# Kernel tuning notes

Measured on AMD Instinct MI355X. Metric: run time of the kernel, lower is better.

The kernel has to match this reference:

```python
import jax, jax.numpy as jnp
import numpy as np

EPS = 1e-12
SMOOTH = 9.0
SGR_STEPS = 3


def l2norm(x, axis=-1):
    return x / jnp.maximum(jnp.linalg.norm(x, axis=axis, keepdims=True), EPS)


def setup_inputs() -> dict:
    key = jax.random.key(0)
    d, s = 1024, 256
    n_img, n_cap, L, n_tok = 64, 64, 32, 197  # 197 -> CLS + 14x14 grid

    def xavier(k, shape):
        lim = float(np.sqrt(6.0 / (shape[-2] + shape[-1])))
        return jax.random.uniform(k, shape, jnp.float32, -lim, lim)

    ks = iter(jax.random.split(key, 32))
    inp = {
        "img_embs": jax.random.normal(next(ks), (n_img, n_tok, d), jnp.float32),
        "cap_embs": jax.random.normal(next(ks), (n_cap, L, d), jnp.float32),
        # constant lengths == max length so the vectorized reference matches
        # the original per-caption loop exactly
        "cap_lens": jnp.full((n_cap,), L, dtype=jnp.int32),
        # visual GlobalSelfAttention
        "vG_Wl": xavier(next(ks), (d, d)), "vG_bl": jnp.zeros((d,), jnp.float32),
        "vG_Wg": xavier(next(ks), (d, d)), "vG_bg": jnp.zeros((d,), jnp.float32),
        "vG_Wc": xavier(next(ks), (d, 1)), "vG_bc": jnp.zeros((1,), jnp.float32),
        # textual GlobalSelfAttention
        "tG_Wl": xavier(next(ks), (d, d)), "tG_bl": jnp.zeros((d,), jnp.float32),
        "tG_Wg": xavier(next(ks), (d, d)), "tG_bg": jnp.zeros((d,), jnp.float32),
        "tG_Wc": xavier(next(ks), (d, 1)), "tG_bc": jnp.zeros((1,), jnp.float32),
        # similarity projections
        "W_loc": xavier(next(ks), (d, s)), "b_loc": jnp.zeros((s,), jnp.float32),
        "W_glo": xavier(next(ks), (d, s)), "b_glo": jnp.zeros((s,), jnp.float32),
        "W_eval": xavier(next(ks), (s, 1)), "b_eval": jnp.zeros((1,), jnp.float32),
        # 3 stacked GraphReasoning layers
        "sgr_Wq": xavier(next(ks), (SGR_STEPS, s, s)), "sgr_bq": jnp.zeros((SGR_STEPS, s), jnp.float32),
        "sgr_Wk": xavier(next(ks), (SGR_STEPS, s, s)), "sgr_bk": jnp.zeros((SGR_STEPS, s), jnp.float32),
        "sgr_Wg": xavier(next(ks), (SGR_STEPS, s, s)), "sgr_bg": jnp.zeros((SGR_STEPS, s), jnp.float32),
    }
    return inp


def global_self_attention(local, raw_global, Wl, bl, Wg, bg, Wc, bc):
    # local: (B, N, d), raw_global: (B, d); dropout is identity at eval
    le = jnp.tanh(local @ Wl + bl)
    ge = jnp.tanh(raw_global @ Wg + bg)
    logits = ((le * ge[:, None, :]) @ Wc + bc)[..., 0]  # (B, N)
    weights = jax.nn.softmax(logits, axis=1)
    global_feat = jnp.sum(weights[..., None] * local, axis=1)
    return l2norm(global_feat, axis=-1)


def scan_attention(query, context, smooth=SMOOTH):
    # query: (B, Nq, d), context: (B, Nc, d)
    attn = jnp.einsum("bcd,bqd->bcq", context, query)
    attn = jax.nn.leaky_relu(attn, negative_slope=0.1)
    attn = l2norm(attn, axis=2)                    # normalize over query dim
    attn = jnp.swapaxes(attn, 1, 2)                # (B, Nq, Nc)
    attn = jax.nn.softmax(attn * smooth, axis=2)   # softmax over context
    weighted = jnp.einsum("bqc,bcd->bqd", attn, context)
    return l2norm(weighted, axis=-1)


def graph_reasoning(sim_emb, Wq, bq, Wk, bk, Wg, bg):
    q = sim_emb @ Wq + bq
    k = sim_emb @ Wk + bk
    edge = jax.nn.softmax(jnp.einsum("bnd,bmd->bnm", q, k), axis=-1)
    sgr = jnp.einsum("bnm,bmd->bnd", edge, sim_emb)
    return jax.nn.relu(sgr @ Wg + bg)


def reference(img_embs, cap_embs, cap_lens,
              vG_Wl, vG_bl, vG_Wg, vG_bg, vG_Wc, vG_bc,
              tG_Wl, tG_bl, tG_Wg, tG_bg, tG_Wc, tG_bc,
              W_loc, b_loc, W_glo, b_glo, W_eval, b_eval,
              sgr_Wq, sgr_bq, sgr_Wk, sgr_bk, sgr_Wg, sgr_bg):
    # 197 tokens -> strip CLS (has_cls_token is True)
    img_tokens = img_embs[:, 1:, :]                      # (n_img, 196, d)
    n_img = img_tokens.shape[0]
    img_avg = img_tokens.mean(axis=1)
    img_global = global_self_attention(img_tokens, img_avg,
                                       vG_Wl, vG_bl, vG_Wg, vG_bg, vG_Wc, vG_bc)

    def per_caption(cap_i):                              # cap_i: (L, d)
        L, d = cap_i.shape
        cap_e = jnp.broadcast_to(cap_i[None], (n_img, L, d))
        cap_avg = jnp.broadcast_to(cap_i.mean(axis=0)[None], (n_img, d))
        cap_global = global_self_attention(cap_e, cap_avg,
                                           tG_Wl, tG_bl, tG_Wg, tG_bg, tG_Wc, tG_bc)
        ctx = scan_attention(cap_e, img_tokens)          # (n_img, L, d)
        sim_loc = l2norm((ctx - cap_e) ** 2 @ W_loc + b_loc, axis=-1)
        sim_glo = l2norm((img_global - cap_global) ** 2 @ W_glo + b_glo, axis=-1)
        sim_emb = jnp.concatenate([sim_glo[:, None, :], sim_loc], axis=1)
        for t in range(SGR_STEPS):
            sim_emb = graph_reasoning(sim_emb, sgr_Wq[t], sgr_bq[t],
                                      sgr_Wk[t], sgr_bk[t], sgr_Wg[t], sgr_bg[t])
        return jax.nn.sigmoid(sim_emb[:, 0, :] @ W_eval + b_eval)[:, 0]  # (n_img,)

    sims = jax.vmap(per_caption)(cap_embs)               # (n_cap, n_img)
    return sims.T                                        # (n_img, n_cap)
```

## Files before the change

### kernel.cpp

```cpp
#include <hip/hip_runtime.h>
#include <hip/hip_bf16.h>
#include <math.h>

#define NI 64
#define NC 64
#define NTOK 197
#define TT 196
#define CL 32
#define DD 1024
#define SS 256
#define NN 33
#define EPSN 1e-12f
#define SMOOTHF 9.0f
#define TP 224

typedef __attribute__((ext_vector_type(8))) short bfrag;
typedef __attribute__((ext_vector_type(4))) float f32x4;
#define MFMA(a, b, c) __builtin_amdgcn_mfma_f32_16x16x32_bf16((a), (b), (c), 0, 0, 0)

#define OFF_ATTNT  0
#define OFF_WTILE  14848
#define OFF_WMAX   23552
#define OFF_NRMS   24064
#define OFF_SEA    0
#define OFF_R1     25344
#define OFF_EB     34560
#define OFF_WKQ    41472
#define OFF_VBUF   42496
#define OFF_QN     42640
#define OFF_RNQ    43152
#define SMEM_BYTES 43280

__device__ __forceinline__ float warp_reduce_sum64(float v) {
#pragma unroll
  for (int m = 32; m > 0; m >>= 1) v += __shfl_xor(v, m, 64);
  return v;
}
__device__ __forceinline__ unsigned short f2b(float f) {
  __hip_bfloat16 h = __float2bfloat16(f);
  return *reinterpret_cast<unsigned short*>(&h);
}
__device__ __forceinline__ float b2f(unsigned short u) {
  union { unsigned int i; float f; } v;
  v.i = ((unsigned int)u) << 16;
  return v.f;
}

__global__ void k_avg(const float* __restrict__ img, const float* __restrict__ cap,
                      float* __restrict__ img_avg, float* __restrict__ cap_avg) {
  int bid = blockIdx.x;
  int tid = threadIdx.x;
  if (bid < NI) {
    int b = bid;
    for (int d = tid; d < DD; d += 256) {
      float acc = 0.f;
      const float* p = img + ((size_t)b * NTOK + 1) * DD + d;
      for (int t = 0; t < TT; ++t) acc += p[(size_t)t * DD];
      img_avg[b * DD + d] = acc * (1.0f / TT);
    }
  } else {
    int c = bid - NI;
    for (int d = tid; d < DD; d += 256) {
      float acc = 0.f;
      const float* p = cap + (size_t)c * CL * DD + d;
      for (int t = 0; t < CL; ++t) acc += p[(size_t)t * DD];
      cap_avg[c * DD + d] = acc * (1.0f / CL);
    }
  }
}

__global__ void k_hvec(const float* __restrict__ avg, const float* __restrict__ Wg,
                       const float* __restrict__ bg, const float* __restrict__ Wc,
                       float* __restrict__ h) {
  __shared__ float av[DD];
  int b = blockIdx.x >> 2;
  int dc = blockIdx.x & 3;
  int tid = threadIdx.x;
  for (int i = tid; i < DD; i += 256) av[i] = avg[b * DD + i];
  __syncthreads();
  int d = dc * 256 + tid;
  float acc = 0.f;
  for (int k = 0; k < DD; k += 4) {
    float4 a4 = *(const float4*)&av[k];
    acc += a4.x * Wg[(size_t)(k + 0) * DD + d];
    acc += a4.y * Wg[(size_t)(k + 1) * DD + d];
    acc += a4.z * Wg[(size_t)(k + 2) * DD + d];
    acc += a4.w * Wg[(size_t)(k + 3) * DD + d];
  }
  h[b * DD + d] = tanhf(acc + bg[d]) * Wc[d];
}

__global__ void k_logits_mfma(const unsigned short* __restrict__ Abf, int rowsPerBatch,
                              const unsigned short* __restrict__ WT,
                              const float* __restrict__ bl, const float* __restrict__ h,
                              float* __restrict__ partial) {
  int tid = threadIdx.x;
  int lane = tid & 63, w = tid >> 6;
  int lrow = lane & 15, lk = (lane >> 4) * 8, rsub = (lane >> 4) * 4;
  int rb = blockIdx.x * 64, c0 = blockIdx.y * 64;
  const unsigned short* ap = Abf + (size_t)(rb + w * 16 + lrow) * DD;
  f32x4 acc[4] = {};
  for (int k0 = 0; k0 < DD; k0 += 32) {
    bfrag a = *(const bfrag*)(ap + k0 + lk);
#pragma unroll
    for (int i = 0; i < 4; ++i) {
      bfrag bb = *(const bfrag*)(WT + (size_t)(c0 + i * 16 + lrow) * DD + k0 + lk);
      acc[i] = MFMA(a, bb, acc[i]);
    }
  }
#pragma unroll
  for (int r = 0; r < 4; ++r) {
    int row = rb + w * 16 + rsub + r;
    int bb2 = row / rowsPerBatch;
    float s = 0.f;
#pragma unroll
    for (int i = 0; i < 4; ++i) {
      int col = c0 + i * 16 + lrow;
      s += tanhf(acc[i][r] + bl[col]) * h[bb2 * DD + col];
    }
    s += __shfl_xor(s, 1, 64);
    s += __shfl_xor(s, 2, 64);
    s += __shfl_xor(s, 4, 64);
    s += __shfl_xor(s, 8, 64);
    if (lrow == 0) partial[(size_t)row * 16 + blockIdx.y] = s;
  }
}

__global__ void k_finish_global(const float* __restrict__ partial, const float* __restrict__ bc,
                                const float* __restrict__ Xbase, long batchStride, int R,
                                float* __restrict__ outG) {
  __shared__ float w[200];
  __shared__ float red[8];
  int b = blockIdx.x, tid = threadIdx.x;
  for (int t = tid; t < R; t += 256) {
    const float* pp = &partial[((size_t)b * R + t) * 16];
    float s = bc[0];
#pragma unroll
    for (int u = 0; u < 16; ++u) s += pp[u];
    w[t] = s;
  }
  __syncthreads();
  float m = -1e30f;
  for (int t = tid; t < R; t += 256) m = fmaxf(m, w[t]);
#pragma unroll
  for (int mm = 32; mm; mm >>= 1) m = fmaxf(m, __shfl_xor(m, mm, 64));
  if ((tid & 63) == 0) red[tid >> 6] = m;
  __syncthreads();
  m = fmaxf(fmaxf(red[0], red[1]), fmaxf(red[2], red[3]));
  __syncthreads();
  for (int t = tid; t < R; t += 256) w[t] = expf(w[t] - m);
  __syncthreads();
  const float* xb = Xbase + (size_t)b * batchStride;
  float acc[4];
  float ss = 0.f;
#pragma unroll
  for (int c4 = 0; c4 < 4; ++c4) {
    int d = tid + c4 * 256;
    float a = 0.f;
    for (int t = 0; t < R; ++t) a += w[t] * xb[(size_t)t * DD + d];
    acc[c4] = a;
    ss += a * a;
  }
  ss = warp_reduce_sum64(ss);
  if ((tid & 63) == 0) red[tid >> 6] = ss;
  __syncthreads();
  ss = red[0] + red[1] + red[2] + red[3];
  float rn = 1.0f / fmaxf(sqrtf(ss), EPSN);
#pragma unroll
  for (int c4 = 0; c4 < 4; ++c4) outG[(size_t)b * DD + tid + c4 * 256] = acc[c4] * rn;
}

__global__ void k_simglo(const float* __restrict__ ig, const float* __restrict__ cg,
                         const float* __restrict__ W, const float* __restrict__ bgl,
                         float* __restrict__ simglo) {
  __shared__ float a_lds[32][20];
  __shared__ float b_lds[32][260];
  int tid = threadIdx.x;
  int p0 = blockIdx.x * 16;
  int ty = tid >> 6, tx = tid & 63;
  int s_rr = tid >> 3, s_kq = tid & 7;
  float acc[4][4] = {};
  for (int k0 = 0; k0 < DD; k0 += 32) {
    float d2[4] = {};
    if (tid < 128) {
      int p = p0 + s_rr;
      int b = p >> 6, c = p & 63;
      float4 giv = *(const float4*)&ig[b * DD + k0 + s_kq * 4];
      float4 cgv = *(const float4*)&cg[c * DD + k0 + s_kq * 4];
      float dx = giv.x - cgv.x, dy = giv.y - cgv.y, dz = giv.z - cgv.z, dw = giv.w - cgv.w;
      d2[0] = dx * dx; d2[1] = dy * dy; d2[2] = dz * dz; d2[3] = dw * dw;
    }
    float4 wv[8];
#pragma unroll
    for (int u = 0; u < 8; ++u)
      wv[u] = *(const float4*)&W[(size_t)(k0 + s_rr) * SS + s_kq * 32 + u * 4];
    __syncthreads();
    if (tid < 128) {
#pragma unroll
      for (int u = 0; u < 4; ++u) a_lds[s_kq * 4 + u][s_rr] = d2[u];
    }
#pragma unroll
    for (int u = 0; u < 8; ++u)
      *(float4*)&b_lds[s_rr][s_kq * 32 + u * 4] = wv[u];
    __syncthreads();
#pragma unroll
    for (int kk = 0; kk < 32; ++kk) {
      float4 a4 = *(const float4*)&a_lds[kk][ty * 4];
      float4 b4 = *(const float4*)&b_lds[kk][tx * 4];
      float av[4] = {a4.x, a4.y, a4.z, a4.w};
      float bv[4] = {b4.x, b4.y, b4.z, b4.w};
#pragma unroll
      for (int i = 0; i < 4; ++i)
#pragma unroll
        for (int j = 0; j < 4; ++j) acc[i][j] += av[i] * bv[j];
    }
  }
#pragma unroll
  for (int i = 0; i < 4; ++i) {
    float v[4];
    float ssq = 0.f;
#pragma unroll
    for (int j = 0; j < 4; ++j) {
      v[j] = acc[i][j] + bgl[tx * 4 + j];
      ssq += v[j] * v[j];
    }
    ssq = warp_reduce_sum64(ssq);
    float rn = 1.0f / fmaxf(sqrtf(ssq), EPSN);
    int p = p0 + ty * 4 + i;
    *(float4*)&simglo[(size_t)p * SS + tx * 4] =
        make_float4(v[0] * rn, v[1] * rn, v[2] * rn, v[3] * rn);
  }
}

__global__ void k_mmatb(const float* __restrict__ Wa, const float* __restrict__ Wb,
                        unsigned short* __restrict__ M) {
  __shared__ float a_lds[32][68];
  __shared__ float b_lds[32][68];
  int tid = threadIdx.x;
  int t = blockIdx.x >> 4;
  int dt = (blockIdx.x >> 2) & 3, et = blockIdx.x & 3;
  int d0 = dt * 64, e0 = et * 64;
  const float* wq = Wa + (size_t)t * SS * SS;
  const float* wk = Wb + (size_t)t * SS * SS;
  int ty = tid >> 4, tx = tid & 15;
  int s_rr = tid >> 2, s_kq = tid & 3;
  float acc[4][4] = {};
  for (int j0 = 0; j0 < SS; j0 += 32) {
    float4 q0 = *(const float4*)&wq[(size_t)(d0 + s_rr) * SS + j0 + s_kq * 8];
    float4 q1 = *(const float4*)&wq[(size_t)(d0 + s_rr) * SS + j0 + s_kq * 8 + 4];
    float4 k0v = *(const float4*)&wk[(size_t)(e0 + s_rr) * SS + j0 + s_kq * 8];
    float4 k1v = *(const float4*)&wk[(size_t)(e0 + s_rr) * SS + j0 + s_kq * 8 + 4];
    __syncthreads();
    float qa[8] = {q0.x, q0.y, q0.z, q0.w, q1.x, q1.y, q1.z, q1.w};
    float ka[8] = {k0v.x, k0v.y, k0v.z, k0v.w, k1v.x, k1v.y, k1v.z, k1v.w};
#pragma unroll
    for (int u = 0; u < 8; ++u) {
      a_lds[s_kq * 8 + u][s_rr] = qa[u];
      b_lds[s_kq * 8 + u][s_rr] = ka[u];
    }
    __syncthreads();
#pragma unroll
    for (int kk = 0; kk < 32; ++kk) {
      float4 a4 = *(const float4*)&a_lds[kk][ty * 4];
      float4 b4 = *(const float4*)&b_lds[kk][tx * 4];
      float av[4] = {a4.x, a4.y, a4.z, a4.w};
      float bv[4] = {b4.x, b4.y, b4.z, b4.w};
#pragma unroll
      for (int i = 0; i < 4; ++i)
#pragma unroll
        for (int j = 0; j < 4; ++j) acc[i][j] += av[i] * bv[j];
    }
  }
#pragma unroll
  for (int i = 0; i < 4; ++i) {
    unsigned int lo = (unsigned int)f2b(acc[i][0]) | ((unsigned int)f2b(acc[i][1]) << 16);
    unsigned int hi = (unsigned int)f2b(acc[i][2]) | ((unsigned int)f2b(acc[i][3]) << 16);
    uint2 o = make_uint2(lo, hi);
    *(uint2*)(M + (size_t)t * SS * SS + (size_t)(d0 + ty * 4 + i) * SS + e0 + tx * 4) = o;
  }
}

__global__ void k_wkbq(const float* __restrict__ Wk, const float* __restrict__ bq,
                       float* __restrict__ out) {
  __shared__ float bv[SS];
  int t = blockIdx.x, tid = threadIdx.x;
  const float* wk = Wk + (size_t)t * SS * SS;
  bv[tid] = bq[t * SS + tid];
  __syncthreads();
  float acc = 0.f;
  for (int j = 0; j < SS; j += 4) {
    float4 wv = *(const float4*)&wk[(size_t)tid * SS + j];
    float4 b4 = *(const float4*)&bv[j];
    acc += wv.x * b4.x + wv.y * b4.y + wv.z * b4.z + wv.w * b4.w;
  }
  out[t * SS + tid] = acc;
}

__global__ void k_imgprep(const float* __restrict__ img, unsigned short* __restrict__ row_bf,
                          unsigned short* __restrict__ tr_bf) {
  __shared__ float t[32][33];
  int b = blockIdx.z;
  int t0 = blockIdx.y * 32, d0 = blockIdx.x * 32;
  int tx = threadIdx.x & 31, ty = threadIdx.x >> 5;
#pragma unroll
  for (int u = 0; u < 4; ++u) {
    int tt = t0 + ty + u * 8;
    float v = (tt < TT) ? img[((size_t)b * NTOK + 1 + tt) * DD + d0 + tx] : 0.f;
    t[ty + u * 8][tx] = v;
    if (tt < TT) row_bf[((size_t)b * TT + tt) * DD + d0 + tx] = f2b(v);
  }
  __syncthreads();
#pragma unroll
  for (int u = 0; u < 4; ++u)
    tr_bf[((size_t)b * DD + d0 + ty + u * 8) * TP + t0 + tx] = f2b(t[tx][ty + u * 8]);
}

__global__ void k_gram_mfma(const unsigned short* __restrict__ img_bf,
                            unsigned short* __restrict__ gram) {
  int tid = threadIdx.x;
  int lane = tid & 63, w = tid >> 6;
  int lrow = lane & 15, lk = (lane >> 4) * 8, rsub = (lane >> 4) * 4;
  int bimg = blockIdx.x;
  int rb = blockIdx.y * 64, cb = blockIdx.z * 64;
  const unsigned short* X = img_bf + (size_t)bimg * TT * DD;
  int ra = rb + w * 16 + lrow;
  if (ra > TT - 1) ra = TT - 1;
  f32x4 acc[4] = {};
  for (int k0 = 0; k0 < DD; k0 += 32) {
    bfrag a = *(const bfrag*)(X + (size_t)ra * DD + k0 + lk);
#pragma unroll
    for (int i = 0; i < 4; ++i) {
      int cc = cb + i * 16 + lrow;
      if (cc > TT - 1) cc = TT - 1;
      bfrag bb = *(const bfrag*)(X + (size_t)cc * DD + k0 + lk);
      acc[i] = MFMA(a, bb, acc[i]);
    }
  }
  unsigned short* Gp = gram + (size_t)bimg * 208 * TP;
#pragma unroll
  for (int i = 0; i < 4; ++i) {
    int cc = cb + i * 16 + lrow;
#pragma unroll
    for (int r = 0; r < 4; ++r) {
      int rr = rb + w * 16 + rsub + r;
      if (rr < 208 && cc < TP)
        Gp[(size_t)rr * TP + cc] = (rr < TT && cc < TT) ? f2b(acc[i][r]) : 0;
    }
  }
}

__global__ void k_castb(const float* __restrict__ s, unsigned short* __restrict__ d, int n4) {
  int i = blockIdx.x * 256 + threadIdx.x;
  if (i < n4) {
    float4 v = *(const float4*)(s + (size_t)i * 4);
    uint2 o;
    o.x = (unsigned int)f2b(v.x) | ((unsigned int)f2b(v.y) << 16);
    o.y = (unsigned int)f2b(v.z) | ((unsigned int)f2b(v.w) << 16);
    *(uint2*)(d + (size_t)i * 4) = o;
  }
}

__global__ void k_tcast(const float* __restrict__ src, unsigned short* __restrict__ dst,
                        int R, int C, long sB, long dB) {
  __shared__ float t[32][33];
  const float* s = src + (size_t)blockIdx.z * sB;
  unsigned short* d = dst + (size_t)blockIdx.z * dB;
  int r0 = blockIdx.y * 32, c0 = blockIdx.x * 32;
  int tx = threadIdx.x & 31, ty = threadIdx.x >> 5;
#pragma unroll
  for (int u = 0; u < 4; ++u)
    t[ty + u * 8][tx] = s[(size_t)(r0 + ty + u * 8) * C + c0 + tx];
  __syncthreads();
#pragma unroll
  for (int u = 0; u < 4; ++u)
    d[(size_t)(c0 + ty + u * 8) * R + r0 + tx] = f2b(t[tx][ty + u * 8]);
}

__global__ __launch_bounds__(256, 3) void k_pair(
    const float* __restrict__ b_loc, const float* __restrict__ simglo,
    const float* __restrict__ wkbq, const float* __restrict__ bg3,
    const float* __restrict__ W_eval, const float* __restrict__ b_eval,
    const unsigned short* __restrict__ cap_bf, const unsigned short* __restrict__ img_bf,
    const unsigned short* __restrict__ imgT_bf, const unsigned short* __restrict__ gram_bf,
    const unsigned short* __restrict__ wlocT_bf, const unsigned short* __restrict__ mt_bf,
    const unsigned short* __restrict__ wgT_bf, float* __restrict__ out) {
  extern __shared__ char smem[];

  int tid = threadIdx.x;
  int lane = tid & 63, w = tid >> 6;
  int lrow = lane & 15;
  int lk = (lane >> 4) * 8;
  int rsub = (lane >> 4) * 4;
  int p = blockIdx.x;
  int b = p >> 6, c = p & 63;
  const unsigned short* imgR = img_bf + (size_t)b * TT * DD;
  const unsigned short* capB = cap_bf + (size_t)c * CL * DD;
  char* attnT_b = smem + OFF_ATTNT;

  {
    f32x4 acc[4][2] = {};
    for (int k0 = 0; k0 < DD; k0 += 32) {
      bfrag bq0 = *(const bfrag*)(capB + (size_t)lrow * DD + k0 + lk);
      bfrag bq1 = *(const bfrag*)(capB + (size_t)(16 + lrow) * DD + k0 + lk);
#pragma unroll
      for (int i = 0; i < 4; ++i) {
        int tt = w + 4 * i;
        if (tt < 13) {
          int t = tt * 16 + lrow;
          bfrag a = {0, 0, 0, 0, 0, 0, 0, 0};
          if (t < TT) a = *(const bfrag*)(imgR + (size_t)t * DD + k0 + lk);
          acc[i][0] = MFMA(a, bq0, acc[i][0]);
          acc[i][1] = MFMA(a, bq1, acc[i][1]);
        }
      }
    }
    float mx0 = -1e30f, mx1 = -1e30f;
#pragma unroll
    for (int i = 0; i < 4; ++i) {
      int tt = w + 4 * i;
      if (tt < 13) {
#pragma unroll
        for (int r = 0; r < 4; ++r) {
          int t = tt * 16 + rsub + r;
          float v0 = acc[i][0][r];
          v0 = v0 < 0.f ? 0.1f * v0 : v0;
          float v1 = acc[i][1][r];
          v1 = v1 < 0.f ? 0.1f * v1 : v1;
          float s2 = v0 * v0 + v1 * v1;
          s2 += __shfl_xor(s2, 1, 64);
          s2 += __shfl_xor(s2, 2, 64);
          s2 += __shfl_xor(s2, 4, 64);
          s2 += __shfl_xor(s2, 8, 64);
          float rn = 1.0f / fmaxf(sqrtf(s2), EPSN);
          v0 *= rn;
          v1 *= rn;
          acc[i][0][r] = v0;
          acc[i][1][r] = v1;
          if (t < TT) {
            mx0 = fmaxf(mx0, v0);
            mx1 = fmaxf(mx1, v1);
          }
        }
      }
    }
    mx0 = fmaxf(mx0, __shfl_xor(mx0, 16, 64));
    mx0 = fmaxf(mx0, __shfl_xor(mx0, 32, 64));
    mx1 = fmaxf(mx1, __shfl_xor(mx1, 16, 64));
    mx1 = fmaxf(mx1, __shfl_xor(mx1, 32, 64));
    float* wmax = (float*)(smem + OFF_WMAX);
    if ((lane >> 4) == 0) {
      wmax[w * 32 + lrow] = mx0;
      wmax[w * 32 + 16 + lrow] = mx1;
    }
    __syncthreads();
    mx0 = fmaxf(fmaxf(wmax[lrow], wmax[32 + lrow]), fmaxf(wmax[64 + lrow], wmax[96 + lrow]));
    mx1 = fmaxf(fmaxf(wmax[16 + lrow], wmax[48 + lrow]),
                fmaxf(wmax[80 + lrow], wmax[112 + lrow]));
#pragma unroll
    for (int i = 0; i < 4; ++i) {
      int tt = w + 4 * i;
#pragma unroll
      for (int r = 0; r < 4; ++r) {
        int t = tt * 16 + rsub + r;
        if (t < TP) {
          unsigned short e0 = 0, e1 = 0;
          if (t < TT) {
            e0 = f2b(expf(SMOOTHF * (acc[i][0][r] - mx0)));
            e1 = f2b(expf(SMOOTHF * (acc[i][1][r] - mx1)));
          }
          *(unsigned short*)(attnT_b + lrow * 464 + t * 2) = e0;
          *(unsigned short*)(attnT_b + (16 + lrow) * 464 + t * 2) = e1;
        }
      }
    }
  }
  __syncthreads();

  {
    float* qn = (float*)(smem + OFF_QN);
    float* nrmS = (float*)(smem + OFF_NRMS);
    const unsigned short* gb = gram_bf + (size_t)b * 208 * TP;
    float part0 = 0.f, part1 = 0.f;
#pragma unroll
    for (int i = 0; i < 4; ++i) {
      int tt = w + 4 * i;
      if (tt < 13) {
        f32x4 y0 = {0.f, 0.f, 0.f, 0.f}, y1 = {0.f, 0.f, 0.f, 0.f};
        for (int t0 = 0; t0 < TP; t0 += 32) {
          bfrag a = *(const bfrag*)(gb + (size_t)(tt * 16 + lrow) * TP + t0 + lk);
          bfrag b0 = *(const bfrag*)(attnT_b + lrow * 464 + (t0 + lk) * 2);
          bfrag b1 = *(const bfrag*)(attnT_b + (16 + lrow) * 464 + (t0 + lk) * 2);
          y0 = MFMA(a, b0, y0);
          y1 = MFMA(a, b1, y1);
        }
#pragma unroll
        for (int r = 0; r < 4; ++r) {
          int t = tt * 16 + rsub + r;
          if (t < TT) {
            part0 += y0[r] * b2f(*(const unsigned short*)(attnT_b + lrow * 464 + t * 2));
            part1 += y1[r] * b2f(*(const unsigned short*)(attnT_b + (16 + lrow) * 464 + t * 2));
          }
        }
      }
    }
    part0 += __shfl_xor(part0, 16, 64);
    part0 += __shfl_xor(part0, 32, 64);
    part1 += __shfl_xor(part1, 16, 64);
    part1 += __shfl_xor(part1, 32, 64);
    if ((lane >> 4) == 0) {
      qn[w * 32 + lrow] = part0;
      qn[w * 32 + 16 + lrow] = part1;
    }
    __syncthreads();
    if (tid < 32)
      nrmS[tid] = 1.0f / fmaxf(sqrtf(qn[tid] + qn[32 + tid] + qn[64 + tid] + qn[96 + tid]), EPSN);
    __syncthreads();
  }

  f32x4 accW[2][4] = {};
  {
    char* wtile_b = smem + OFF_WTILE;
    float* nrmS = (float*)(smem + OFF_NRMS);
    float nrm0 = nrmS[lrow], nrm1 = nrmS[16 + lrow];
    for (int d0 = 0; d0 < DD; d0 += 128) {
      f32x4 c2[2][2] = {};
      for (int t0 = 0; t0 < TP; t0 += 32) {
        bfrag b0 = *(const bfrag*)(attnT_b + lrow * 464 + (t0 + lk) * 2);
        bfrag b1 = *(const bfrag*)(attnT_b + (16 + lrow) * 464 + (t0 + lk) * 2);
#pragma unroll
        for (int i = 0; i < 2; ++i) {
          int dt = w + 4 * i;
          bfrag a = *(const bfrag*)(imgT_bf + ((size_t)b * DD + d0 + dt * 16 + lrow) * TP + t0 + lk);
          c2[i][0] = MFMA(a, b0, c2[i][0]);
          c2[i][1] = MFMA(a, b1, c2[i][1]);
        }
      }
      __syncthreads();
#pragma unroll
      for (int i = 0; i < 2; ++i) {
        int dl = (w + 4 * i) * 16 + rsub;
#pragma unroll
        for (int qt = 0; qt < 2; ++qt) {
          int q = qt * 16 + lrow;
          uint2 cu = *(const uint2*)(capB + (size_t)q * DD + d0 + dl);
          float cf0 = b2f(cu.x & 0xffff), cf1 = b2f(cu.x >> 16);
          float cf2 = b2f(cu.y & 0xffff), cf3 = b2f(cu.y >> 16);
          float rn = qt ? nrm1 : nrm0;
          float v0 = c2[i][qt][0] * rn - cf0;
          float v1 = c2[i][qt][1] * rn - cf1;
          float v2 = c2[i][qt][2] * rn - cf2;
          float v3 = c2[i][qt][3] * rn - cf3;
          unsigned int lo = (unsigned int)f2b(v0 * v0) | ((unsigned int)f2b(v1 * v1) << 16);
          unsigned int hi = (unsigned int)f2b(v2 * v2) | ((unsigned int)f2b(v3 * v3) << 16);
          *(uint2*)(wtile_b + q * 272 + dl * 2) = make_uint2(lo, hi);
        }
      }
      __syncthreads();
      for (int kc = 0; kc < 4; ++kc) {
        bfrag a0 = *(const bfrag*)(wtile_b + lrow * 272 + (kc * 32 + lk) * 2);
        bfrag a1 = *(const bfrag*)(wtile_b + (16 + lrow) * 272 + (kc * 32 + lk) * 2);
#pragma unroll
        for (int sti = 0; sti < 4; ++sti) {
          int s = (w * 4 + sti) * 16 + lrow;
          bfrag bb = *(const bfrag*)(wlocT_bf + (size_t)s * DD + d0 + kc * 32 + lk);
          accW[0][sti] = MFMA(a0, bb, accW[0][sti]);
          accW[1][sti] = MFMA(a1, bb, accW[1][sti]);
        }
      }
    }
  }

  {
    char* seA_b = smem + OFF_SEA;
    float* qn = (float*)(smem + OFF_QN);
    float* rnq = (float*)(smem + OFF_RNQ);
    __syncthreads();
    for (int i2 = tid; i2 < 6336; i2 += 256) ((unsigned int*)smem)[i2] = 0;
    __syncthreads();
    float blv[4];
#pragma unroll
    for (int sti = 0; sti < 4; ++sti) blv[sti] = b_loc[(w * 4 + sti) * 16 + lrow];
    float ss[2][4];
#pragma unroll
    for (int qt = 0; qt < 2; ++qt)
#pragma unroll
      for (int r = 0; r < 4; ++r) {
        float s2 = 0.f;
#pragma unroll
        for (int sti = 0; sti < 4; ++sti) {
          float v = accW[qt][sti][r] + blv[sti];
          s2 += v * v;
        }
        s2 += __shfl_xor(s2, 1, 64);
        s2 += __shfl_xor(s2, 2, 64);
        s2 += __shfl_xor(s2, 4, 64);
        s2 += __shfl_xor(s2, 8, 64);
        ss[qt][r] = s2;
      }
    if (lrow == 0) {
#pragma unroll
      for (int qt = 0; qt < 2; ++qt)
#pragma unroll
        for (int r = 0; r < 4; ++r)
          qn[w * 32 + qt * 16 + rsub + r] = ss[qt][r];
    }
    __syncthreads();
    if (tid < 32)
      rnq[tid] = 1.0f / fmaxf(sqrtf(qn[tid] + qn[32 + tid] + qn[64 + tid] + qn[96 + tid]), EPSN);
    __syncthreads();
#pragma unroll
    for (int qt = 0; qt < 2; ++qt)
#pragma unroll
      for (int r = 0; r < 4; ++r) {
        int q = qt * 16 + rsub + r;
        float rn = rnq[q];
#pragma unroll
        for (int sti = 0; sti < 4; ++sti) {
          int s = (w * 4 + sti) * 16 + lrow;
          float v = (accW[qt][sti][r] + blv[sti]) * rn;
          *(unsigned short*)(seA_b + (1 + q) * 528 + s * 2) = f2b(v);
        }
      }
    if (tid < 64) {
      float4 g4 = *(const float4*)&simglo[(size_t)p * SS + tid * 4];
      unsigned int lo = (unsigned int)f2b(g4.x) | ((unsigned int)f2b(g4.y) << 16);
      unsigned int hi = (unsigned int)f2b(g4.z) | ((unsigned int)f2b(g4.w) << 16);
      *(uint2*)(seA_b + tid * 8) = make_uint2(lo, hi);
    }
    __syncthreads();
  }

  {
    char* seA_b = smem + OFF_SEA;
    char* Gc_b = smem + OFF_R1;
    char* XT_b = smem + OFF_R1;
    float* Ef = (float*)(smem + OFF_R1);
    char* Eb = smem + OFF_EB;
    float* wkq = (float*)(smem + OFF_WKQ);
    float* vbuf = (float*)(smem + OFF_VBUF);

    for (int step = 0; step < 3; ++step) {
      const unsigned short* mstep = mt_bf + (size_t)step * SS * SS;
      const unsigned short* wstep = wgT_bf + (size_t)step * SS * SS;
      wkq[tid] = wkbq[step * SS + tid];
      __syncthreads();
      if (tid < 132) {
        int m = tid >> 2, qq = tid & 3;
        float a = 0.f;
        for (int e = qq * 64; e < qq * 64 + 64; e += 2) {
          unsigned int u = *(const unsigned int*)(seA_b + m * 528 + e * 2);
          a += b2f(u & 0xffff) * wkq[e] + b2f(u >> 16) * wkq[e + 1];
        }
        a += __shfl_xor(a, 1, 64);
        a += __shfl_xor(a, 2, 64);
        if (qq == 0) vbuf[m] = a;
      }
      f32x4 aE[3] = {};
      for (int ec = 0; ec < 4; ++ec) {
        f32x4 aGc[3] = {};
        for (int kc = 0; kc < 8; ++kc) {
          int k = kc * 32 + lk;
          bfrag bb = *(const bfrag*)(mstep + (size_t)(ec * 64 + w * 16 + lrow) * SS + k);
#pragma unroll
          for (int mt = 0; mt < 3; ++mt) {
            bfrag af = *(const bfrag*)(seA_b + (mt * 16 + lrow) * 528 + k * 2);
            aGc[mt] = MFMA(af, bb, aGc[mt]);
          }
        }
        __syncthreads();
#pragma unroll
        for (int mt = 0; mt < 3; ++mt)
#pragma unroll
          for (int r = 0; r < 4; ++r)
            *(unsigned short*)(Gc_b + (mt * 16 + rsub + r) * 144 + (w * 16 + lrow) * 2) =
                f2b(aGc[mt][r]);
        __syncthreads();
#pragma unroll
        for (int kc = 0; kc < 2; ++kc) {
          int k = kc * 32 + lk;
#pragma unroll
          for (int ti = 0; ti < 3; ++ti) {
            int tile = w + ti * 4;
            if (tile < 9) {
              int mtE = tile / 3, ntE = tile - mtE * 3;
              bfrag ga = *(const bfrag*)(Gc_b + (mtE * 16 + lrow) * 144 + k * 2);
              bfrag sb = *(const bfrag*)(seA_b + (ntE * 16 + lrow) * 528 + (ec * 64 + k) * 2);
              aE[ti] = MFMA(ga, sb, aE[ti]);
            }
          }
        }
      }
      __syncthreads();
#pragma unroll
      for (int ti = 0; ti < 3; ++ti) {
        int tile = w + ti * 4;
        if (tile < 9) {
          int mtE = tile / 3, ntE = tile - mtE * 3;
          int n0 = mtE * 16 + rsub, m = ntE * 16 + lrow;
#pragma unroll
          for (int r = 0; r < 4; ++r)
            if (n0 + r < NN && m < NN) Ef[(n0 + r) * 34 + m] = aE[ti][r] + vbuf[m];
        }
      }
      __syncthreads();
      if (tid < NN) {
        float mx = -1e30f;
        for (int mm = 0; mm < NN; ++mm) mx = fmaxf(mx, Ef[tid * 34 + mm]);
        float sum = 0.f;
        for (int mm = 0; mm < NN; ++mm) {
          float e = expf(Ef[tid * 34 + mm] - mx);
          Ef[tid * 34 + mm] = e;
          sum += e;
        }
        float rs = 1.0f / sum;
        for (int mm = 0; mm < NN; ++mm) Ef[tid * 34 + mm] *= rs;
      }
      __syncthreads();
      for (int idx = tid; idx < 48 * 36; idx += 256) {
        int n = idx / 36, mp = (idx - n * 36) * 2;
        unsigned int lo = (n < NN && mp < NN) ? (unsigned int)f2b(Ef[n * 34 + mp]) : 0u;
        unsigned int hi = (n < NN && mp + 1 < NN) ? (unsigned int)f2b(Ef[n * 34 + mp + 1]) : 0u;
        *(unsigned int*)(Eb + n * 144 + mp * 2) = lo | (hi << 16);
      }
      __syncthreads();
      unsigned int oPk[4][3][2];
#pragma unroll
      for (int sc = 0; sc < 4; ++sc) {
        f32x4 aX[3] = {};
        for (int kc = 0; kc < 8; ++kc) {
          int k = kc * 32 + lk;
          bfrag bb = *(const bfrag*)(wstep + (size_t)(sc * 64 + w * 16 + lrow) * SS + k);
#pragma unroll
          for (int mt = 0; mt < 3; ++mt) {
            bfrag af = *(const bfrag*)(seA_b + (mt * 16 + lrow) * 528 + k * 2);
            aX[mt] = MFMA(af, bb, aX[mt]);
          }
        }
        __syncthreads();
#pragma unroll
        for (int mt = 0; mt < 3; ++mt) {
          unsigned int lo = (unsigned int)f2b(aX[mt][0]) | ((unsigned int)f2b(aX[mt][1]) << 16);
          unsigned int hi = (unsigned int)f2b(aX[mt][2]) | ((unsigned int)f2b(aX[mt][3]) << 16);
          *(uint2*)(XT_b + (w * 16 + lrow) * 144 + (mt * 16 + rsub) * 2) = make_uint2(lo, hi);
        }
        *(uint2*)(XT_b + (w * 16 + lrow) * 144 + (48 + rsub) * 2) = make_uint2(0, 0);
        __syncthreads();
        f32x4 aO[3] = {};
#pragma unroll
        for (int kc = 0; kc < 2; ++kc) {
          int k = kc * 32 + lk;
          bfrag xa = *(const bfrag*)(XT_b + (w * 16 + lrow) * 144 + k * 2);
#pragma unroll
          for (int nt = 0; nt < 3; ++nt) {
            bfrag eb = *(const bfrag*)(Eb + (nt * 16 + lrow) * 144 + k * 2);
            aO[nt] = MFMA(xa, eb, aO[nt]);
          }
        }
        float bga[4];
#pragma unroll
        for (int r = 0; r < 4; ++r) bga[r] = bg3[step * SS + sc * 64 + w * 16 + rsub + r];
#pragma unroll
        for (int nt = 0; nt < 3; ++nt) {
          float v0 = fmaxf(aO[nt][0] + bga[0], 0.f);
          float v1 = fmaxf(aO[nt][1] + bga[1], 0.f);
          float v2 = fmaxf(aO[nt][2] + bga[2], 0.f);
          float v3 = fmaxf(aO[nt][3] + bga[3], 0.f);
          oPk[sc][nt][0] = (unsigned int)f2b(v0) | ((unsigned int)f2b(v1) << 16);
          oPk[sc][nt][1] = (unsigned int)f2b(v2) | ((unsigned int)f2b(v3) << 16);
        }
      }
#pragma unroll
      for (int sc = 0; sc < 4; ++sc)
#pragma unroll
        for (int nt = 0; nt < 3; ++nt) {
          int n = nt * 16 + lrow;
          if (n < NN)
            *(uint2*)(seA_b + n * 528 + (sc * 64 + w * 16 + rsub) * 2) =
                make_uint2(oPk[sc][nt][0], oPk[sc][nt][1]);
        }
      __syncthreads();
    }
  }

  if (tid < 64) {
    const char* seA_b = smem + OFF_SEA;
    uint2 u = *(const uint2*)(seA_b + tid * 8);
    float4 w4 = *(const float4*)&W_eval[tid * 4];
    float s = b2f(u.x & 0xffff) * w4.x + b2f(u.x >> 16) * w4.y +
              b2f(u.y & 0xffff) * w4.z + b2f(u.y >> 16) * w4.w;
    s = warp_reduce_sum64(s);
    if (tid == 0) out[b * 64 + c] = 1.0f / (1.0f + expf(-(s + b_eval[0])));
  }
}

extern "C" void kernel_launch(void* const* d_in, const int* in_sizes, int n_in,
                              void* d_out, int out_size, void* d_ws, size_t ws_size,
                              hipStream_t stream) {
  (void)in_sizes; (void)n_in; (void)out_size; (void)ws_size;
  const float* img = (const float*)d_in[0];
  const float* cap = (const float*)d_in[1];
  const float* vG_Wl = (const float*)d_in[3];
  const float* vG_bl = (const float*)d_in[4];
  const float* vG_Wg = (const float*)d_in[5];
  const float* vG_bg = (const float*)d_in[6];
  const float* vG_Wc = (const float*)d_in[7];
  const float* vG_bc = (const float*)d_in[8];
  const float* tG_Wl = (const float*)d_in[9];
  const float* tG_bl = (const float*)d_in[10];
  const float* tG_Wg = (const float*)d_in[11];
  const float* tG_bg = (const float*)d_in[12];
  const float* tG_Wc = (const float*)d_in[13];
  const float* tG_bc = (const float*)d_in[14];
  const float* W_loc = (const float*)d_in[15];
  const float* b_loc = (const float*)d_in[16];
  const float* W_glo = (const float*)d_in[17];
  const float* b_glo = (const float*)d_in[18];
  const float* W_eval = (const float*)d_in[19];
  const float* b_eval = (const float*)d_in[20];
  const float* sgr_Wq = (const float*)d_in[21];
  const float* sgr_bq = (const float*)d_in[22];
  const float* sgr_Wk = (const float*)d_in[23];
  const float* sgr_Wg = (const float*)d_in[25];
  const float* sgr_bg = (const float*)d_in[26];
  float* out = (float*)d_out;
  float* ws = (float*)d_ws;
  float* img_avg = ws;
  float* cap_avg = ws + 65536;
  float* h_img = ws + 131072;
  float* h_cap = ws + 196608;
  float* part_img = ws + 262144;
  float* part_cap = ws + 462848;
  float* img_glob = ws + 495616;
  float* cap_glob = ws + 561152;
  float* simglo = ws + 626688;
  float* wkbqv = ws + 1675264;
  unsigned short* ub = (unsigned short*)(ws + 1676032);
  unsigned short* mt_bf = ub;
  unsigned short* wgT_bf = ub + 196608;
  unsigned short* wlocT_bf = ub + 393216;
  unsigned short* cap_bf = ub + 655360;
  unsigned short* gram_bf = ub + 2752512;
  unsigned short* imgT_bf = ub + 5734400;
  unsigned short* img_bf = ub + 20414464;
  unsigned short* wlT_v = ub + 33259520;
  unsigned short* wlT_t = ub + 34308096;

  k_avg<<<128, 256, 0, stream>>>(img, cap, img_avg, cap_avg);
  k_hvec<<<256, 256, 0, stream>>>(img_avg, vG_Wg, vG_bg, vG_Wc, h_img);
  k_hvec<<<256, 256, 0, stream>>>(cap_avg, tG_Wg, tG_bg, tG_Wc, h_cap);
  k_imgprep<<<dim3(32, 7, 64), 256, 0, stream>>>(img, img_bf, imgT_bf);
  k_castb<<<2048, 256, 0, stream>>>(cap, cap_bf, 524288);
  k_tcast<<<dim3(32, 32, 1), 256, 0, stream>>>(vG_Wl, wlT_v, 1024, 1024, 0, 0);
  k_tcast<<<dim3(32, 32, 1), 256, 0, stream>>>(tG_Wl, wlT_t, 1024, 1024, 0, 0);
  k_logits_mfma<<<dim3(196, 16), 256, 0, stream>>>(img_bf, TT, wlT_v, vG_bl, h_img, part_img);
  k_logits_mfma<<<dim3(32, 16), 256, 0, stream>>>(cap_bf, CL, wlT_t, tG_bl, h_cap, part_cap);
  k_finish_global<<<64, 256, 0, stream>>>(part_img, vG_bc, img + DD, (long)NTOK * DD, TT,
                                          img_glob);
  k_finish_global<<<64, 256, 0, stream>>>(part_cap, tG_bc, cap, (long)CL * DD, CL, cap_glob);
  k_simglo<<<256, 256, 0, stream>>>(img_glob, cap_glob, W_glo, b_glo, simglo);
  k_mmatb<<<48, 256, 0, stream>>>(sgr_Wk, sgr_Wq, mt_bf);
  k_wkbq<<<3, 256, 0, stream>>>(sgr_Wk, sgr_bq, wkbqv);
  k_gram_mfma<<<dim3(64, 4, 4), 256, 0, stream>>>(img_bf, gram_bf);
  k_tcast<<<dim3(8, 8, 3), 256, 0, stream>>>(sgr_Wg, wgT_bf, 256, 256, 65536, 65536);
  k_tcast<<<dim3(8, 32, 1), 256, 0, stream>>>(W_loc, wlocT_bf, 1024, 256, 0, 0);
  hipFuncSetAttribute((const void*)k_pair, hipFuncAttributeMaxDynamicSharedMemorySize,
                      SMEM_BYTES);
  k_pair<<<4096, 256, SMEM_BYTES, stream>>>(b_loc, simglo, wkbqv, sgr_bg, W_eval, b_eval,
                                            cap_bf, img_bf, imgT_bf, gram_bf, wlocT_bf,
                                            mt_bf, wgT_bf, out);
}
```

Baseline: 1.953 ms.

## Merge logits/finish launches, shrink k_pair shared memory for higher occupancy

```diff
diff --git a/kernel.cpp b/kernel.cpp
--- a/kernel.cpp
+++ b/kernel.cpp
@@ -22,14 +22,14 @@
 #define OFF_WTILE  14848
 #define OFF_WMAX   23552
 #define OFF_NRMS   24064
+#define OFF_QN     25344
+#define OFF_RNQ    25856
 #define OFF_SEA    0
-#define OFF_R1     25344
-#define OFF_EB     34560
-#define OFF_WKQ    41472
-#define OFF_VBUF   42496
-#define OFF_QN     42640
-#define OFF_RNQ    43152
-#define SMEM_BYTES 43280
+#define OFF_EB     25344
+#define OFF_R1     30096
+#define OFF_WKQ    37008
+#define OFF_VBUF   38032
+#define SMEM_BYTES 39312
 
 __device__ __forceinline__ float warp_reduce_sum64(float v) {
 #pragma unroll
@@ -90,14 +90,28 @@
   h[b * DD + d] = tanhf(acc + bg[d]) * Wc[d];
 }
 
-__global__ void k_logits_mfma(const unsigned short* __restrict__ Abf, int rowsPerBatch,
-                              const unsigned short* __restrict__ WT,
-                              const float* __restrict__ bl, const float* __restrict__ h,
-                              float* __restrict__ partial) {
+__global__ void k_logits2(const unsigned short* __restrict__ Ai, const unsigned short* __restrict__ Wi,
+                          const float* __restrict__ bli, const float* __restrict__ hi,
+                          float* __restrict__ pi,
+                          const unsigned short* __restrict__ Ac, const unsigned short* __restrict__ Wc2,
+                          const float* __restrict__ blc, const float* __restrict__ hc,
+                          float* __restrict__ pc) {
   int tid = threadIdx.x;
   int lane = tid & 63, w = tid >> 6;
   int lrow = lane & 15, lk = (lane >> 4) * 8, rsub = (lane >> 4) * 4;
-  int rb = blockIdx.x * 64, c0 = blockIdx.y * 64;
+  int bx = blockIdx.x;
+  const unsigned short* Abf;
+  const unsigned short* WT;
+  const float* bl;
+  const float* h;
+  float* partial;
+  int rb, rowsPerBatch;
+  if (bx < 196) {
+    Abf = Ai; WT = Wi; bl = bli; h = hi; partial = pi; rb = bx * 64; rowsPerBatch = TT;
+  } else {
+    Abf = Ac; WT = Wc2; bl = blc; h = hc; partial = pc; rb = (bx - 196) * 64; rowsPerBatch = CL;
+  }
+  int c0 = blockIdx.y * 64;
   const unsigned short* ap = Abf + (size_t)(rb + w * 16 + lrow) * DD;
   f32x4 acc[4] = {};
   for (int k0 = 0; k0 < DD; k0 += 32) {
@@ -126,12 +140,24 @@
   }
 }
 
-__global__ void k_finish_global(const float* __restrict__ partial, const float* __restrict__ bc,
-                                const float* __restrict__ Xbase, long batchStride, int R,
-                                float* __restrict__ outG) {
+__global__ void k_finish2(const float* __restrict__ pi, const float* __restrict__ bci,
+                          const float* __restrict__ Xi, long bsi, int Ri, float* __restrict__ oi,
+                          const float* __restrict__ pc, const float* __restrict__ bcc,
+                          const float* __restrict__ Xc, long bsc, int Rc, float* __restrict__ oc) {
   __shared__ float w[200];
   __shared__ float red[8];
-  int b = blockIdx.x, tid = threadIdx.x;
+  int bid = blockIdx.x, tid = threadIdx.x;
+  const float* partial;
+  const float* bc;
+  const float* Xbase;
+  long batchStride;
+  int R, b;
+  float* outG;
+  if (bid < 64) {
+    partial = pi; bc = bci; Xbase = Xi; batchStride = bsi; R = Ri; outG = oi; b = bid;
+  } else {
+    partial = pc; bc = bcc; Xbase = Xc; batchStride = bsc; R = Rc; outG = oc; b = bid - 64;
+  }
   for (int t = tid; t < R; t += 256) {
     const float* pp = &partial[((size_t)b * R + t) * 16];
     float s = bc[0];
@@ -376,7 +402,7 @@
     d[(size_t)(c0 + ty + u * 8) * R + r0 + tx] = f2b(t[tx][ty + u * 8]);
 }
 
-__global__ __launch_bounds__(256, 3) void k_pair(
+__global__ __launch_bounds__(256, 4) void k_pair(
     const float* __restrict__ b_loc, const float* __restrict__ simglo,
     const float* __restrict__ wkbq, const float* __restrict__ bg3,
     const float* __restrict__ W_eval, const float* __restrict__ b_eval,
@@ -716,10 +742,10 @@
         for (int mm = 0; mm < NN; ++mm) Ef[tid * 34 + mm] *= rs;
       }
       __syncthreads();
-      for (int idx = tid; idx < 48 * 36; idx += 256) {
+      for (int idx = tid; idx < 33 * 36; idx += 256) {
         int n = idx / 36, mp = (idx - n * 36) * 2;
-        unsigned int lo = (n < NN && mp < NN) ? (unsigned int)f2b(Ef[n * 34 + mp]) : 0u;
-        unsigned int hi = (n < NN && mp + 1 < NN) ? (unsigned int)f2b(Ef[n * 34 + mp + 1]) : 0u;
+        unsigned int lo = (mp < NN) ? (unsigned int)f2b(Ef[n * 34 + mp]) : 0u;
+        unsigned int hi = (mp + 1 < NN) ? (unsigned int)f2b(Ef[n * 34 + mp + 1]) : 0u;
         *(unsigned int*)(Eb + n * 144 + mp * 2) = lo | (hi << 16);
       }
       __syncthreads();
@@ -852,11 +878,10 @@
   k_castb<<<2048, 256, 0, stream>>>(cap, cap_bf, 524288);
   k_tcast<<<dim3(32, 32, 1), 256, 0, stream>>>(vG_Wl, wlT_v, 1024, 1024, 0, 0);
   k_tcast<<<dim3(32, 32, 1), 256, 0, stream>>>(tG_Wl, wlT_t, 1024, 1024, 0, 0);
-  k_logits_mfma<<<dim3(196, 16), 256, 0, stream>>>(img_bf, TT, wlT_v, vG_bl, h_img, part_img);
-  k_logits_mfma<<<dim3(32, 16), 256, 0, stream>>>(cap_bf, CL, wlT_t, tG_bl, h_cap, part_cap);
-  k_finish_global<<<64, 256, 0, stream>>>(part_img, vG_bc, img + DD, (long)NTOK * DD, TT,
-                                          img_glob);
-  k_finish_global<<<64, 256, 0, stream>>>(part_cap, tG_bc, cap, (long)CL * DD, CL, cap_glob);
+  k_logits2<<<dim3(228, 16), 256, 0, stream>>>(img_bf, wlT_v, vG_bl, h_img, part_img,
+                                               cap_bf, wlT_t, tG_bl, h_cap, part_cap);
+  k_finish2<<<128, 256, 0, stream>>>(part_img, vG_bc, img + DD, (long)NTOK * DD, TT, img_glob,
+                                     part_cap, tG_bc, cap, (long)CL * DD, CL, cap_glob);
   k_simglo<<<256, 256, 0, stream>>>(img_glob, cap_glob, W_glo, b_glo, simglo);
   k_mmatb<<<48, 256, 0, stream>>>(sgr_Wk, sgr_Wq, mt_bf);
   k_wkbq<<<3, 256, 0, stream>>>(sgr_Wk, sgr_bq, wkbqv);
```

New measurement: 1.826 ms. 6.5% less time.
